# Kernel tuning notes

Hardware: AMD Instinct MI355X
Metric: run time of the kernel (lower is better)

## Reference

```python
import jax, jax.numpy as jnp
import numpy as np

D_MODEL = 2048
N_HEADS = 16
D_K = D_MODEL // N_HEADS
MAX_SEQ_LEN = 2048


def _rotary_tables(dim, max_seq_len):
    angular_freq = (1.0 / 10000.0) ** jnp.linspace(0.0, 1.0, dim // 2, dtype=jnp.float32)
    t = jnp.arange(max_seq_len, dtype=jnp.float32)
    theta = jnp.einsum('i,j->ij', t, angular_freq)  # [S, dk/2]
    return jnp.cos(theta), jnp.sin(theta)


def _apply_rotary(x, cos, sin):
    # x: [B, H, S, dk]; cos/sin: [S, dk/2]
    seq_len = x.shape[-2]
    c = cos[:seq_len][None, None]
    s = sin[:seq_len][None, None]
    x1, x2 = jnp.split(x, 2, axis=-1)
    y1 = x1 * c - x2 * s
    y2 = x1 * s + x2 * c
    return jnp.concatenate([y1, y2], axis=-1).astype(x.dtype)


def setup_inputs() -> dict:
    key = jax.random.key(0)
    k_x, k_qkv, k_o = jax.random.split(key, 3)
    B, S = 2, 2048
    x = jax.random.normal(k_x, (B, S, D_MODEL), dtype=jnp.float32)
    scale = 1.0 / np.sqrt(D_MODEL)
    w_qkv = jax.random.normal(k_qkv, (3 * D_MODEL, D_MODEL), dtype=jnp.float32) * scale
    w_o = jax.random.normal(k_o, (D_MODEL, D_MODEL), dtype=jnp.float32) * scale
    return {"x": x, "w_qkv": w_qkv, "w_o": w_o}


def reference(x, w_qkv, w_o):
    B, S, _ = x.shape
    cos, sin = _rotary_tables(D_K, MAX_SEQ_LEN)
    qkv = jnp.einsum('bsd,ed->bse', x, w_qkv)  # [B, S, 3*d_model]
    qkv = qkv.reshape(B, S, 3, N_HEADS, D_K).transpose(2, 0, 3, 1, 4)  # [3,B,H,S,dk]
    Q, K, V = qkv[0], qkv[1], qkv[2]
    Q = _apply_rotary(Q, cos, sin)
    K = _apply_rotary(K, cos, sin)
    scale = 1.0 / np.sqrt(D_K)
    scores = jnp.einsum('bhqd,bhkd->bhqk', Q, K) * scale
    causal = jnp.tril(jnp.ones((S, S), dtype=bool))
    scores = jnp.where(causal[None, None], scores, jnp.finfo(scores.dtype).min)
    attn = jax.nn.softmax(scores, axis=-1)
    out = jnp.einsum('bhqk,bhkd->bhqd', attn, V)  # [B,H,S,dk]
    out = out.transpose(0, 2, 1, 3).reshape(B, S, D_MODEL)
    return jnp.einsum('bsd,ed->bse', out, w_o)
```

## Files before the change

kernel.cpp:

```cpp
#include <hip/hip_runtime.h>
#include <hip/hip_bf16.h>


typedef __bf16 bf16;
typedef __bf16 bf16x4 __attribute__((ext_vector_type(4)));
typedef __bf16 bf16x8 __attribute__((ext_vector_type(8)));
typedef float f32x4 __attribute__((ext_vector_type(4)));
typedef float f32x16 __attribute__((ext_vector_type(16)));
typedef int i32x4 __attribute__((ext_vector_type(4)));

#define DEV __device__ __forceinline__

DEV void gll16(const void* g, void* lds_base_wave_uniform) {
  __builtin_amdgcn_global_load_lds((const __attribute__((address_space(1))) void*)g,
                                   (__attribute__((address_space(3))) void*)lds_base_wave_uniform,
                                   16, 0, 0);
}

DEV f32x4 mfma16(bf16x8 a, bf16x8 b, f32x4 c) {
  return __builtin_amdgcn_mfma_f32_16x16x32_bf16(a, b, c, 0, 0, 0);
}
DEV f32x16 mfma32(bf16x8 a, bf16x8 b, f32x16 c) {
  return __builtin_amdgcn_mfma_f32_32x32x16_bf16(a, b, c, 0, 0, 0);
}

DEV int pack2(float x, float y) {
  union { bf16 h[2]; int i; } u;
  u.h[0] = (bf16)x; u.h[1] = (bf16)y;
  return u.i;
}

__global__ __launch_bounds__(256) void cvt_f32_bf16(const float* __restrict__ in,
                                                    bf16* __restrict__ out, int n) {
  int i = (blockIdx.x * 256 + threadIdx.x) << 3;
  if (i >= n) return;
  float4 a = *(const float4*)(in + i);
  float4 b = *(const float4*)(in + i + 4);
  bf16x8 o;
  o[0] = (bf16)a.x; o[1] = (bf16)a.y; o[2] = (bf16)a.z; o[3] = (bf16)a.w;
  o[4] = (bf16)b.x; o[5] = (bf16)b.y; o[6] = (bf16)b.z; o[7] = (bf16)b.w;
  *(bf16x8*)(out + i) = o;
}

__global__ __launch_bounds__(256) void rope_table(float* __restrict__ ctab,
                                                  float* __restrict__ stab) {
  int id = blockIdx.x * 256 + threadIdx.x;
  int s = id >> 6, j = id & 63;
  float freq = powf(10000.0f, -(float)j / 63.0f);
  float th = (float)s * freq;
  ctab[id] = cosf(th);
  stab[id] = sinf(th);
}

__global__ __launch_bounds__(256) void rope_apply(bf16* __restrict__ Qb, bf16* __restrict__ Kb,
                                                  const float* __restrict__ ctab,
                                                  const float* __restrict__ stab) {
  const float QSCALE = 0.08838834764831845f * 1.4426950408889634f;
  int id = blockIdx.x * 256 + threadIdx.x;
  const int half = 32 * 2048 * 8;
  bf16* P = (id < half) ? Qb : Kb;
  const float scale = (id < half) ? QSCALE : 1.0f;
  int t = (id < half) ? id : id - half;
  const int d0 = (t & 7) << 3;
  const int s = (t >> 3) & 2047;
  const int bh = t >> 14;
  bf16* p = P + (((size_t)bh * 2048 + s) << 7);
  bf16x8 x1 = *(bf16x8*)(p + d0);
  bf16x8 x2 = *(bf16x8*)(p + d0 + 64);
  float4 ca = *(const float4*)(ctab + (s << 6) + d0);
  float4 cb = *(const float4*)(ctab + (s << 6) + d0 + 4);
  float4 sa = *(const float4*)(stab + (s << 6) + d0);
  float4 sb = *(const float4*)(stab + (s << 6) + d0 + 4);
  const float c[8] = {ca.x, ca.y, ca.z, ca.w, cb.x, cb.y, cb.z, cb.w};
  const float sn[8] = {sa.x, sa.y, sa.z, sa.w, sb.x, sb.y, sb.z, sb.w};
  bf16x8 y1, y2;
#pragma unroll
  for (int j = 0; j < 8; ++j) {
    const float a = (float)x1[j], b = (float)x2[j];
    y1[j] = (bf16)((a * c[j] - b * sn[j]) * scale);
    y2[j] = (bf16)((a * sn[j] + b * c[j]) * scale);
  }
  *(bf16x8*)(p + d0) = y1;
  *(bf16x8*)(p + d0 + 64) = y2;
}

template <int NTN, int MODE>
__global__ __launch_bounds__(512, 4) void gemm_p(const bf16* __restrict__ A,
                                                 const bf16* __restrict__ Bt,
                                                 bf16* __restrict__ q_out,
                                                 bf16* __restrict__ k_out,
                                                 bf16* __restrict__ v_out,
                                                 float* __restrict__ f_out) {
  constexpr int K = 2048, NKT = K / 32;
  constexpr int BUFB = 24576;
  __shared__ bf16 lds[3 * 12288];
  const int nwg = NTN * 32;
  const int id = blockIdx.x;
  const int swz = (id & 7) * (nwg >> 3) + (id >> 3);
  const int bx = swz % NTN, by = swz / NTN;
  const int m0 = by << 7, n0 = bx << 8;
  const int tid = threadIdx.x, w = tid >> 6, l = tid & 63;
  const int wm = w >> 2, wn = w & 3;

  const int lsl = (l & 7) ^ ((l >> 3) & 7);
  const int srow = ((l >> 3) << 1) + (lsl >> 2);
  const int scol = (lsl & 3) << 3;

  auto STAGE = [&](int t, char* base) {
    const int k0 = t << 5;
    {
      const int row = (w << 4) + srow;
      gll16(A + (size_t)(m0 + row) * K + k0 + scol, base + (w << 10));
    }
#pragma unroll
    for (int s2 = 0; s2 < 2; ++s2) {
      const int row = (s2 << 7) + (w << 4) + srow;
      gll16(Bt + (size_t)(n0 + row) * K + k0 + scol, base + 8192 + (s2 << 13) + (w << 10));
    }
  };

  f32x4 acc[4][4] = {};

  STAGE(0, (char*)lds);
  STAGE(1, (char*)lds + BUFB);
  asm volatile("s_waitcnt vmcnt(3)" ::: "memory");
  __builtin_amdgcn_s_barrier();

#pragma unroll 1
  for (int t = 0, bi = 0, bj = 2; t < NKT; ++t) {
    char* rbase = (char*)lds + bi * BUFB;
    bf16x8 af[4], bfr[4];
#pragma unroll
    for (int i = 0; i < 4; ++i) {
      const int row = (wm << 6) + (i << 4) + (l & 15);
      const int sr = row >> 1;
      af[i] = *(const bf16x8*)(rbase + sr * 128 +
                               (((((row & 1) << 2) | (l >> 4)) ^ (sr & 7)) << 4));
    }
#pragma unroll
    for (int j = 0; j < 4; ++j) {
      const int row = (wn << 6) + (j << 4) + (l & 15);
      const int sr = row >> 1;
      bfr[j] = *(const bf16x8*)(rbase + 8192 + sr * 128 +
                                (((((row & 1) << 2) | (l >> 4)) ^ (sr & 7)) << 4));
    }
    if (t + 2 < NKT) STAGE(t + 2, (char*)lds + bj * BUFB);
    asm volatile("s_waitcnt lgkmcnt(0)" ::: "memory");
    __builtin_amdgcn_s_setprio(1);
#pragma unroll
    for (int i = 0; i < 4; ++i)
#pragma unroll
      for (int j = 0; j < 4; ++j)
        acc[i][j] = mfma16(af[i], bfr[j], acc[i][j]);
    __builtin_amdgcn_s_setprio(0);
    if (t + 2 < NKT) {
      asm volatile("s_waitcnt vmcnt(3)" ::: "memory");
    } else if (t + 2 == NKT) {
      asm volatile("s_waitcnt vmcnt(0)" ::: "memory");
    }
    __builtin_amdgcn_sched_barrier(0);
    __builtin_amdgcn_s_barrier();
    bi = (bi == 2) ? 0 : bi + 1;
    bj = (bj == 2) ? 0 : bj + 1;
  }

  if constexpr (MODE == 0) {
    const int which = n0 >> 11;
    const int h = ((n0 + (wn << 6)) >> 7) & 15;
    const int dlo = ((wn & 1) << 6);
    if (which < 2) {
      bf16* dst = which ? k_out : q_out;
#pragma unroll
      for (int i = 0; i < 4; ++i)
#pragma unroll
        for (int j = 0; j < 4; ++j) {
          const int d = dlo + (j << 4) + (l & 15);
#pragma unroll
          for (int r = 0; r < 4; ++r) {
            const int m = m0 + (wm << 6) + (i << 4) + ((l >> 4) << 2) + r;
            const int b_ = m >> 11, s = m & 2047;
            dst[(((size_t)((b_ << 4) | h)) * 2048 + s) * 128 + d] = (bf16)acc[i][j][r];
          }
        }
    } else {
#pragma unroll
      for (int i = 0; i < 4; ++i)
#pragma unroll
        for (int j = 0; j < 4; ++j) {
          const int d = dlo + (j << 4) + (l & 15);
          const int sb = m0 + (wm << 6) + (i << 4) + ((l >> 4) << 2);
          const int b_ = sb >> 11, s = sb & 2047;
          bf16x4 vv;
#pragma unroll
          for (int r = 0; r < 4; ++r) vv[r] = (bf16)acc[i][j][r];
          *(bf16x4*)(v_out + ((size_t)((b_ << 4) | h) << 18) + ((size_t)d << 11) + s) = vv;
        }
    }
  } else {
#pragma unroll
    for (int i = 0; i < 4; ++i)
#pragma unroll
      for (int j = 0; j < 4; ++j)
#pragma unroll
        for (int r = 0; r < 4; ++r) {
          const int m = m0 + (wm << 6) + (i << 4) + ((l >> 4) << 2) + r;
          const int n = n0 + (wn << 6) + (j << 4) + (l & 15);
          f_out[(size_t)m * 2048 + n] = acc[i][j][r];
        }
  }
}

__global__ __launch_bounds__(256, 2) void attn_kernel(const bf16* __restrict__ Qb,
                                                      const bf16* __restrict__ Kb,
                                                      const bf16* __restrict__ Vt,
                                                      bf16* __restrict__ Ao) {
  constexpr int S = 2048;
  __shared__ bf16 Ks[2][64 * 128];
  __shared__ bf16 Vs[2][128 * 64];
  const int idx = blockIdx.x;
  const int bh = idx >> 4;
  int qt = idx & 15;
  if (idx & 256) qt = 15 - qt;
  const int q0 = qt << 7;
  const int tid = threadIdx.x, w = tid >> 6, l = tid & 63;
  const int hi = l >> 5;
  const bf16* Qp = Qb + ((size_t)bh << 18);
  const bf16* Kp = Kb + ((size_t)bh << 18);
  const bf16* Vp = Vt + ((size_t)bh << 18);

  auto STAGE_KV = [&](int kv0, int bufi) {
    char* Kbase = (char*)Ks + (bufi << 14);
    char* Vbase = (char*)Vs + (bufi << 14);
#pragma unroll
    for (int i = 0; i < 4; ++i) {
      const int rk = (w << 4) + (i << 2) + (l >> 4);
      gll16(Kp + ((size_t)(kv0 + rk) << 7) + (((l & 15) ^ (rk & 7)) << 3),
            Kbase + (w << 12) + (i << 10));
      const int rv = (w << 5) + (i << 3) + (l >> 3);
      gll16(Vp + (size_t)rv * S + kv0 + (((l & 7) ^ (rv & 7)) << 3),
            Vbase + (w << 12) + (i << 10));
    }
  };

  bf16x8 qf[8];
#pragma unroll
  for (int kt = 0; kt < 8; ++kt)
    qf[kt] = *(const bf16x8*)(Qp + ((size_t)(q0 + (w << 5) + (l & 31)) << 7) + (kt << 4) + (hi << 3));

  f32x16 o[4] = {};
  float mrun = -3e38f, lrun = 0.f;

  const int qminw = q0 + (w << 5);
  const int qmaxw = qminw + 31;
  const int kv_end = q0 + 128;

  STAGE_KV(0, 0);
  __syncthreads();

  int bufi = 0;
#pragma unroll 1
  for (int kv0 = 0; kv0 < kv_end; kv0 += 64, bufi ^= 1) {
    if (kv0 + 64 < kv_end) STAGE_KV(kv0 + 64, bufi ^ 1);
    if (kv0 <= qmaxw) {
      const char* Kbase = (const char*)Ks + (bufi << 14);
      const char* Vbase = (const char*)Vs + (bufi << 14);
      f32x16 sc0 = {}, sc1 = {};
      __builtin_amdgcn_s_setprio(1);
#pragma unroll
      for (int kt = 0; kt < 8; ++kt) {
        const int rk0 = l & 31;
        const int coff = ((kt << 5) + (hi << 4));
        bf16x8 k0 = *(const bf16x8*)(Kbase + (rk0 << 8) + (coff ^ ((rk0 & 7) << 4)));
        bf16x8 k1 = *(const bf16x8*)(Kbase + ((rk0 + 32) << 8) + (coff ^ ((rk0 & 7) << 4)));
        sc0 = mfma32(k0, qf[kt], sc0);
        sc1 = mfma32(k1, qf[kt], sc1);
      }
      __builtin_amdgcn_s_setprio(0);
      if (kv0 + 63 > qminw) {
        const int qg = qminw + (l & 31);
#pragma unroll
        for (int r = 0; r < 16; ++r) {
          const int kvr = kv0 + (r & 3) + ((r >> 2) << 3) + (hi << 2);
          if (kvr > qg) sc0[r] = -3e38f;
          if (kvr + 32 > qg) sc1[r] = -3e38f;
        }
      }
      float mx = -3e38f;
#pragma unroll
      for (int r = 0; r < 16; ++r) mx = fmaxf(mx, fmaxf(sc0[r], sc1[r]));
      mx = fmaxf(mx, __shfl_xor(mx, 32));
      const float mnew = fmaxf(mrun, mx);
      if (!__all(mx <= mrun)) {
        const float alpha = exp2f(mrun - mnew);
        lrun *= alpha;
#pragma unroll
        for (int dt = 0; dt < 4; ++dt) o[dt] *= alpha;
      }
      mrun = mnew;
      float ps = 0.f;
#pragma unroll
      for (int r = 0; r < 16; ++r) {
        sc0[r] = exp2f(sc0[r] - mnew); ps += sc0[r];
        sc1[r] = exp2f(sc1[r] - mnew); ps += sc1[r];
      }
      ps += __shfl_xor(ps, 32);
      lrun += ps;
#pragma unroll
      for (int ks = 0; ks < 4; ++ks) {
        const f32x16& s = (ks & 2) ? sc1 : sc0;
        const int rb = (ks & 1) << 3;
        int pa_ = pack2(s[rb + 0], s[rb + 1]);
        int pb_ = pack2(s[rb + 2], s[rb + 3]);
        int pc_ = pack2(s[rb + 4], s[rb + 5]);
        int pd_ = pack2(s[rb + 6], s[rb + 7]);
        int sa = __shfl_xor(pa_, 32), sb = __shfl_xor(pb_, 32);
        int sc_ = __shfl_xor(pc_, 32), sd = __shfl_xor(pd_, 32);
        i32x4 pi;
        pi[0] = hi ? sc_ : pa_;
        pi[1] = hi ? sd : pb_;
        pi[2] = hi ? pc_ : sa;
        pi[3] = hi ? pd_ : sb;
        const bf16x8 pf = __builtin_bit_cast(bf16x8, pi);
        __builtin_amdgcn_s_setprio(1);
#pragma unroll
        for (int dt = 0; dt < 4; ++dt) {
          const int rd = (dt << 5) + (l & 31);
          const bf16x8 vf = *(const bf16x8*)(Vbase + (rd << 7) +
                                             (((ks << 5) + (hi << 4)) ^ ((rd & 7) << 4)));
          o[dt] = mfma32(vf, pf, o[dt]);
        }
        __builtin_amdgcn_s_setprio(0);
      }
    }
    __syncthreads();
  }
  const float rinv = 1.0f / lrun;
  const int b = bh >> 4, h = bh & 15;
  const int qg = q0 + (w << 5) + (l & 31);
  bf16* Arow = Ao + (((size_t)(b * S + qg)) << 11) + (h << 7);
#pragma unroll
  for (int dt = 0; dt < 4; ++dt)
#pragma unroll
    for (int g = 0; g < 4; ++g) {
      bf16x4 ov;
#pragma unroll
      for (int r = 0; r < 4; ++r) ov[r] = (bf16)(o[dt][(g << 2) + r] * rinv);
      *(bf16x4*)(Arow + (dt << 5) + (g << 3) + (hi << 2)) = ov;
    }
}

extern "C" void kernel_launch(void* const* d_in, const int* in_sizes, int n_in,
                              void* d_out, int out_size, void* d_ws, size_t ws_size,
                              hipStream_t stream) {
  const float* x = (const float*)d_in[0];
  const float* w_qkv = (const float*)d_in[1];
  const float* w_o = (const float*)d_in[2];
  float* out = (float*)d_out;
  char* ws = (char*)d_ws;

  bf16* xb    = (bf16*)(ws);
  bf16* wqkvb = (bf16*)(ws + (16ull << 20));
  bf16* wob   = (bf16*)(ws + (40ull << 20));
  bf16* Qb    = (bf16*)(ws + (48ull << 20));
  bf16* Kb    = (bf16*)(ws + (64ull << 20));
  bf16* Vt    = (bf16*)(ws + (80ull << 20));
  bf16* Ao    = (bf16*)(ws + (96ull << 20));
  float* ctab = (float*)(ws + (112ull << 20));
  float* stab = (float*)(ws + (113ull << 20));

  cvt_f32_bf16<<<4096, 256, 0, stream>>>(x, xb, 2 * 2048 * 2048);
  cvt_f32_bf16<<<6144, 256, 0, stream>>>(w_qkv, wqkvb, 6144 * 2048);
  cvt_f32_bf16<<<2048, 256, 0, stream>>>(w_o, wob, 2048 * 2048);
  rope_table<<<512, 256, 0, stream>>>(ctab, stab);
  gemm_p<24, 0><<<768, 512, 0, stream>>>(xb, wqkvb, Qb, Kb, Vt, nullptr);
  rope_apply<<<4096, 256, 0, stream>>>(Qb, Kb, ctab, stab);
  attn_kernel<<<512, 256, 0, stream>>>(Qb, Kb, Vt, Ao);
  gemm_p<8, 1><<<256, 512, 0, stream>>>(Ao, wob, nullptr, nullptr, nullptr, out);
}
```

Measured before the change: 277.9 us.

## Use 256x384 macro-tile GEMM for the QKV projection

Adds a dedicated QKV projection kernel with a 256x384 output tile per 512-thread block, a triple-buffered LDS pipeline and 8x6 MFMA accumulators per wave. The launch drops from 768 workgroups of 128x256 to 256 larger ones. The aim is higher arithmetic intensity per LDS/global load and one wave of workgroups across the CUs. In exchange it uses more LDS and registers (launch bounds 2 blocks), which lowers occupancy and can cause spilling.

```diff
diff --git a/kernel.cpp b/kernel.cpp
--- a/kernel.cpp
+++ b/kernel.cpp
@@ -84,6 +84,128 @@
   *(bf16x8*)(p + d0 + 64) = y2;
 }
 
+__global__ __launch_bounds__(512, 2) void gemm384(const bf16* __restrict__ A,
+                                                  const bf16* __restrict__ Bt,
+                                                  bf16* __restrict__ q_out,
+                                                  bf16* __restrict__ k_out,
+                                                  bf16* __restrict__ v_out) {
+  constexpr int K = 2048, NKT = 64;
+  constexpr int BUFB = 40960;
+  __shared__ char lds[3 * BUFB];
+  const int id = blockIdx.x;
+  const int swz = (id & 7) * 32 + (id >> 3);
+  const int bx = swz & 15, by = swz >> 4;
+  const int m0 = by << 8;
+  const int n0 = bx * 384;
+  const int tid = threadIdx.x, w = tid >> 6, l = tid & 63;
+  const int wm = w >> 2, wn = w & 3;
+  const int lsl = (l & 7) ^ ((l >> 3) & 7);
+  const int srow = ((l >> 3) << 1) + (lsl >> 2);
+  const int scol = (lsl & 3) << 3;
+
+  auto STAGE = [&](int t, char* base) {
+    const int k0 = t << 5;
+#pragma unroll
+    for (int c = 0; c < 2; ++c) {
+      const int row = (c << 7) + (w << 4) + srow;
+      gll16(A + (size_t)(m0 + row) * K + k0 + scol, base + (c << 13) + (w << 10));
+    }
+#pragma unroll
+    for (int c = 0; c < 3; ++c) {
+      const int row = (c << 7) + (w << 4) + srow;
+      gll16(Bt + (size_t)(n0 + row) * K + k0 + scol, base + 16384 + (c << 13) + (w << 10));
+    }
+  };
+
+  f32x4 acc[8][6] = {};
+
+  STAGE(0, (char*)lds);
+  STAGE(1, (char*)lds + BUFB);
+  asm volatile("s_waitcnt vmcnt(5)" ::: "memory");
+  __builtin_amdgcn_s_barrier();
+
+#pragma unroll 1
+  for (int t = 0, bi = 0, bj = 2; t < NKT; ++t) {
+    char* rbase = (char*)lds + bi * BUFB;
+    bf16x8 bfr[6];
+#pragma unroll
+    for (int j = 0; j < 6; ++j) {
+      const int row = wn * 96 + (j << 4) + (l & 15);
+      const int sr = row >> 1;
+      bfr[j] = *(const bf16x8*)(rbase + 16384 + sr * 128 +
+                                (((((row & 1) << 2) | (l >> 4)) ^ (sr & 7)) << 4));
+    }
+    bf16x8 af[4];
+#pragma unroll
+    for (int i = 0; i < 4; ++i) {
+      const int row = (wm << 7) + (i << 4) + (l & 15);
+      const int sr = row >> 1;
+      af[i] = *(const bf16x8*)(rbase + sr * 128 +
+                               (((((row & 1) << 2) | (l >> 4)) ^ (sr & 7)) << 4));
+    }
+    if (t + 2 < NKT) STAGE(t + 2, (char*)lds + bj * BUFB);
+    asm volatile("s_waitcnt lgkmcnt(0)" ::: "memory");
+    __builtin_amdgcn_sched_barrier(0);
+    __builtin_amdgcn_s_setprio(1);
+#pragma unroll
+    for (int i = 0; i < 4; ++i)
+#pragma unroll
+      for (int j = 0; j < 6; ++j)
+        acc[i][j] = mfma16(af[i], bfr[j], acc[i][j]);
+    __builtin_amdgcn_s_setprio(0);
+#pragma unroll
+    for (int i = 0; i < 4; ++i) {
+      const int row = (wm << 7) + 64 + (i << 4) + (l & 15);
+      const int sr = row >> 1;
+      af[i] = *(const bf16x8*)(rbase + sr * 128 +
+                               (((((row & 1) << 2) | (l >> 4)) ^ (sr & 7)) << 4));
+    }
+    asm volatile("s_waitcnt lgkmcnt(0)" ::: "memory");
+    __builtin_amdgcn_sched_barrier(0);
+    __builtin_amdgcn_s_setprio(1);
+#pragma unroll
+    for (int i = 0; i < 4; ++i)
+#pragma unroll
+      for (int j = 0; j < 6; ++j)
+        acc[4 + i][j] = mfma16(af[i], bfr[j], acc[4 + i][j]);
+    __builtin_amdgcn_s_setprio(0);
+    if (t + 2 < NKT) {
+      asm volatile("s_waitcnt vmcnt(5)" ::: "memory");
+    } else if (t + 2 == NKT) {
+      asm volatile("s_waitcnt vmcnt(0)" ::: "memory");
+    }
+    __builtin_amdgcn_sched_barrier(0);
+    __builtin_amdgcn_s_barrier();
+    bi = (bi == 2) ? 0 : bi + 1;
+    bj = (bj == 2) ? 0 : bj + 1;
+  }
+
+#pragma unroll
+  for (int i = 0; i < 8; ++i)
+#pragma unroll
+    for (int j = 0; j < 6; ++j) {
+      const int nl = n0 + wn * 96 + (j << 4) + (l & 15);
+      const int which = nl >> 11;
+      const int h = (nl >> 7) & 15, d = nl & 127;
+      if (which < 2) {
+        bf16* dst = which ? k_out : q_out;
+#pragma unroll
+        for (int r = 0; r < 4; ++r) {
+          const int m = m0 + (wm << 7) + (i << 4) + ((l >> 4) << 2) + r;
+          const int b_ = m >> 11, s = m & 2047;
+          dst[(((size_t)((b_ << 4) | h)) * 2048 + s) * 128 + d] = (bf16)acc[i][j][r];
+        }
+      } else {
+        const int sb = m0 + (wm << 7) + (i << 4) + ((l >> 4) << 2);
+        const int b_ = sb >> 11, s = sb & 2047;
+        bf16x4 vv;
+#pragma unroll
+        for (int r = 0; r < 4; ++r) vv[r] = (bf16)acc[i][j][r];
+        *(bf16x4*)(v_out + ((size_t)((b_ << 4) | h) << 18) + ((size_t)d << 11) + s) = vv;
+      }
+    }
+}
+
 template <int NTN, int MODE>
 __global__ __launch_bounds__(512, 4) void gemm_p(const bf16* __restrict__ A,
                                                  const bf16* __restrict__ Bt,
@@ -101,7 +223,6 @@
   const int m0 = by << 7, n0 = bx << 8;
   const int tid = threadIdx.x, w = tid >> 6, l = tid & 63;
   const int wm = w >> 2, wn = w & 3;
-
   const int lsl = (l & 7) ^ ((l >> 3) & 7);
   const int srow = ((l >> 3) << 1) + (lsl >> 2);
   const int scol = (lsl & 3) << 3;
@@ -372,7 +493,7 @@
   cvt_f32_bf16<<<6144, 256, 0, stream>>>(w_qkv, wqkvb, 6144 * 2048);
   cvt_f32_bf16<<<2048, 256, 0, stream>>>(w_o, wob, 2048 * 2048);
   rope_table<<<512, 256, 0, stream>>>(ctab, stab);
-  gemm_p<24, 0><<<768, 512, 0, stream>>>(xb, wqkvb, Qb, Kb, Vt, nullptr);
+  gemm384<<<256, 512, 0, stream>>>(xb, wqkvb, Qb, Kb, Vt);
   rope_apply<<<4096, 256, 0, stream>>>(Qb, Kb, ctab, stab);
   attn_kernel<<<512, 256, 0, stream>>>(Qb, Kb, Vt, Ao);
   gemm_p<8, 1><<<256, 512, 0, stream>>>(Ao, wob, nullptr, nullptr, nullptr, out);
```

New measurement: 255.6 us. 8.0% less time.
